# Optimization experiments

Measured on AMD Instinct MI355X. Metric: run time of the kernel, lower is better.

The kernel has to match this reference:

```python
import jax, jax.numpy as jnp
import numpy as np

EPS = 1e-9
C, Hd, Wd = 3, 64, 64  # input_dimensions[1:]

def setup_inputs() -> dict:
    key = jax.random.key(0)
    ks = jax.random.split(key, 8)
    S, B = 8, 512
    num_digits, num_style, num_hidden, bott, num_pixels = 10, 50, 512, 160, C * Hd * Wd
    return {
        "digits": jax.random.uniform(ks[0], (S, B, num_digits), dtype=jnp.float32),
        "styles": jax.random.normal(ks[1], (S, B, num_style), dtype=jnp.float32),
        "images": jax.random.uniform(ks[2], (S, B, C, Hd, Wd), dtype=jnp.float32),
        "W_h": jax.random.normal(ks[3], (num_digits + num_style, num_hidden), dtype=jnp.float32) * 0.05,
        "b_h": jnp.zeros((num_hidden,), jnp.float32),
        "W1": jax.random.normal(ks[4], (num_hidden, bott), dtype=jnp.float32) * 0.05,
        "b1": jnp.zeros((bott,), jnp.float32),
        "W2": jax.random.normal(ks[5], (bott, num_pixels), dtype=jnp.float32) * 0.05,
        "b2": jnp.zeros((num_pixels,), jnp.float32),
    }

def reference(digits, styles, images, W_h, b_h, W1, b1, W2, b2):
    # dec_hidden: Linear + ReLU, fully batched over [S, B]
    h = jax.nn.relu(jnp.concatenate([digits, styles], axis=-1) @ W_h + b_h)  # [S,B,Hn]
    # hidden_pass (original loops per-sample; here a single batched GEMM chain)
    t = jax.nn.selu(h @ W1 + b1)                 # [S,B,160]
    x_hat = jax.nn.sigmoid(t @ W2 + b2)          # [S,B,P]
    S, B, _ = x_hat.shape
    images_mean = x_hat.reshape(S, B, C, Hd, Wd)
    # eps-guarded BCE-style log-likelihood loss, summed over last dim only
    loss = -(jnp.log(images_mean + EPS) * images
             + jnp.log(1.0 - images_mean + EPS) * (1.0 - images)).sum(-1)  # [S,B,C,Hd]
    return loss
```

## Files before the change

kernel.cpp:

```cpp
#include <hip/hip_runtime.h>
#include <hip/hip_bf16.h>
#include <math.h>


#define SELU_SCALE 1.0507009873554804934193349852946f
#define SELU_ALPHA 1.6732632423543772848170429916717f

typedef __attribute__((ext_vector_type(8))) short bf16x8;
typedef __attribute__((ext_vector_type(4))) float f32x4;

static __device__ __forceinline__ short f2bf(float x) {
    __hip_bfloat16 h = __float2bfloat16(x);
    short s;
    __builtin_memcpy(&s, &h, 2);
    return s;
}

__global__ __launch_bounds__(512) void producer_kernel(
    const float* __restrict__ digits,
    const float* __restrict__ styles,
    const float* __restrict__ Wh,
    const float* __restrict__ bh,
    const float* __restrict__ W1,
    const float* __restrict__ b1,
    const float* __restrict__ W2,
    __hip_bfloat16* __restrict__ w2f,
    __hip_bfloat16* __restrict__ tf)
{
    __shared__ __align__(16) char smem[46912];
    const int tid = threadIdx.x;

    if (blockIdx.x < 256) {
        float (*cat_s)[60] = (float(*)[60])smem;
        float* h_s = (float*)(smem + 3840);
        float (*t_s)[161] = (float(*)[161])(smem + 3840 + 32768);
        const int rowBase = blockIdx.x * 16;

        for (int i = tid; i < 16 * 60; i += 512) {
            const int r = i / 60, k = i % 60;
            const int row = rowBase + r;
            cat_s[r][k] = (k < 10) ? digits[row * 10 + k]
                                   : styles[row * 50 + (k - 10)];
        }
        __syncthreads();

        {
            float acc[16];
            const float bias = bh[tid];
#pragma unroll
            for (int r = 0; r < 16; ++r) acc[r] = bias;
            for (int k = 0; k < 60; ++k) {
                const float w = Wh[k * 512 + tid];
#pragma unroll
                for (int r = 0; r < 16; ++r) acc[r] = fmaf(cat_s[r][k], w, acc[r]);
            }
#pragma unroll
            for (int r = 0; r < 16; ++r)
                h_s[r * 512 + tid] = fmaxf(acc[r], 0.0f);
        }
        __syncthreads();

        if (tid < 320) {
            const int rh = (tid >= 160) ? 1 : 0;
            const int col = tid - rh * 160;
            const int r0 = rh * 8;
            float acc[8];
            const float bias = b1[col];
#pragma unroll
            for (int r = 0; r < 8; ++r) acc[r] = bias;

#pragma unroll 4
            for (int k = 0; k < 512; k += 4) {
                const float w0 = W1[(size_t)(k + 0) * 160 + col];
                const float w1 = W1[(size_t)(k + 1) * 160 + col];
                const float w2 = W1[(size_t)(k + 2) * 160 + col];
                const float w3 = W1[(size_t)(k + 3) * 160 + col];
#pragma unroll
                for (int r = 0; r < 8; ++r) {
                    const float4 hv = *(const float4*)&h_s[(r0 + r) * 512 + k];
                    float a = acc[r];
                    a = fmaf(hv.x, w0, a);
                    a = fmaf(hv.y, w1, a);
                    a = fmaf(hv.z, w2, a);
                    a = fmaf(hv.w, w3, a);
                    acc[r] = a;
                }
            }
#pragma unroll
            for (int r = 0; r < 8; ++r) {
                const float z = acc[r];
                const float s = (z > 0.0f) ? (SELU_SCALE * z)
                                           : (SELU_SCALE * SELU_ALPHA * expm1f(z));
                t_s[r0 + r][col] = s;
            }
        }
        __syncthreads();

        if (tid < 320) {
            const int kk = tid >> 6;
            const int l = tid & 63;
            const int lr = l & 15, lh = l >> 4;
            bf16x8 v;
#pragma unroll
            for (int j = 0; j < 8; ++j)
                v[j] = f2bf(t_s[lr][kk * 32 + lh * 8 + j]);
            *(bf16x8*)((short*)tf + ((size_t)blockIdx.x * 5 + kk) * 512 + l * 8) = v;
        }
    } else {
        float (*tile)[64] = (float(*)[64])(smem + (tid >> 8) * 8192);
        const int p = (blockIdx.x - 256) * 2 + (tid >> 8);
        const int t256 = tid & 255;
        const int bx = p / 5, by = p % 5;
        const int colBase = bx * 64;
        const int kBase = by * 32;

        for (int i = t256; i < 32 * 64; i += 256)
            tile[i >> 6][i & 63] =
                W2[(size_t)(kBase + (i >> 6)) * 12288 + colBase + (i & 63)];
        __syncthreads();

        const int c16 = t256 >> 6;
        const int lane = t256 & 63;
        const int lr = lane & 15, lh = lane >> 4;

        bf16x8 v;
#pragma unroll
        for (int j = 0; j < 8; ++j)
            v[j] = f2bf(tile[lh * 8 + j][c16 * 16 + lr]);

        const size_t chunk = (size_t)(bx * 4 + c16) * 5 + by;
        *(bf16x8*)((short*)w2f + chunk * 512 + lane * 8) = v;
    }
}

__global__ __launch_bounds__(256, 3) void out_loss_mfma_kernel(
    const __hip_bfloat16* __restrict__ tf,
    const __hip_bfloat16* __restrict__ w2f,
    const float* __restrict__ b2,
    const float* __restrict__ images,
    float* __restrict__ out)
{
    __shared__ short w2s[20 * 512];
    __shared__ float ims[4][2048];

    const int tid = threadIdx.x;
    const int lane = tid & 63;
    const int wv = tid >> 6;
    const int rowBase = blockIdx.y * 128 + wv * 32;
    const int colBase = blockIdx.x * 64;
    const int lr = lane & 15;
    const int lh = lane >> 4;

    const short* wfb = (const short*)w2f;
    const short* tfb = (const short*)tf;
    const char* imb = (const char*)images;

    const int r16base = rowBase >> 4;
    bf16x8 bT[5][2];
#pragma unroll
    for (int kk = 0; kk < 5; ++kk)
#pragma unroll
        for (int r = 0; r < 2; ++r)
            bT[kk][r] = *(const bf16x8*)(tfb
                + ((size_t)(r16base + r) * 5 + kk) * 512 + lane * 8);
    float4 bc[4];
#pragma unroll
    for (int c = 0; c < 4; ++c)
        bc[c] = *(const float4*)(b2 + colBase + c * 16 + lh * 4);

    {
        const size_t chunkBase = (size_t)blockIdx.x * 20;
#pragma unroll
        for (int tch = 0; tch < 5; ++tch) {
            const int cw = wv + tch * 4;
            __builtin_amdgcn_global_load_lds(
                (const uint32_t*)(wfb + (chunkBase + cw) * 512 + lane * 8),
                (uint32_t*)&w2s[cw * 512], 16, 0, 0);
        }
    }
    {
        const int rsub = lane >> 4;
        const int m = lane & 15;
#pragma unroll
        for (int w = 0; w < 8; ++w) {
            const int r = w * 4 + rsub;
            const size_t gb = (size_t)(rowBase + r) * 49152 + (size_t)colBase * 4
                            + (size_t)((16 * m) ^ ((r & 15) << 4));
            __builtin_amdgcn_global_load_lds((const uint32_t*)(imb + gb),
                (uint32_t*)&ims[wv][w * 256], 16, 0, 0);
        }
    }

    asm volatile("s_waitcnt vmcnt(8)" ::: "memory");
    __builtin_amdgcn_sched_barrier(0);
    __builtin_amdgcn_s_barrier();

    f32x4 acc[4][2] = {};
#pragma unroll
    for (int kk = 0; kk < 5; ++kk) {
        bf16x8 aW[4];
#pragma unroll
        for (int c = 0; c < 4; ++c)
            aW[c] = *(const bf16x8*)&w2s[(c * 5 + kk) * 512 + lane * 8];
#pragma unroll
        for (int c = 0; c < 4; ++c)
#pragma unroll
            for (int r = 0; r < 2; ++r)
                acc[c][r] = __builtin_amdgcn_mfma_f32_16x16x32_bf16(
                    aW[c], bT[kk][r], acc[c][r], 0, 0, 0);
    }

    const float* myq = ims[wv];
#pragma unroll
    for (int rw = 0; rw < 2; ++rw) {
        if (rw == 0) {
            asm volatile("s_waitcnt vmcnt(4)" ::: "memory");
        } else {
            asm volatile("s_waitcnt vmcnt(0)" ::: "memory");
        }
        __builtin_amdgcn_sched_barrier(0);

        float mx = 0.f;
        float pr = 1.f;
        float zi = 0.f;
#pragma unroll
        for (int c = 0; c < 4; ++c) {
            const int fidx = (rw * 16 + lr) * 64 + ((lh * 4 + c * 16) ^ (lr << 2));
            const float4 im4 = *(const float4*)&myq[fidx];
            const float imv[4] = {im4.x, im4.y, im4.z, im4.w};
            const float bcv[4] = {bc[c].x, bc[c].y, bc[c].z, bc[c].w};
#pragma unroll
            for (int j = 0; j < 4; ++j) {
                const float z = acc[c][rw][j] + bcv[j];
                mx += fmaxf(z, 0.0f);
                pr *= 1.0f + __expf(-fabsf(z));
                zi = fmaf(z, imv[j], zi);
            }
        }
        float part = mx + __logf(pr) - zi;

        part += __shfl_xor(part, 16);
        part += __shfl_xor(part, 32);

        if (lane < 16)
            out[(size_t)(rowBase + rw * 16 + lane) * 192 + blockIdx.x] = part;
    }
}

extern "C" void kernel_launch(void* const* d_in, const int* in_sizes, int n_in,
                              void* d_out, int out_size, void* d_ws, size_t ws_size,
                              hipStream_t stream) {
    const float* digits = (const float*)d_in[0];
    const float* styles = (const float*)d_in[1];
    const float* images = (const float*)d_in[2];
    const float* Wh     = (const float*)d_in[3];
    const float* bh     = (const float*)d_in[4];
    const float* W1     = (const float*)d_in[5];
    const float* b1     = (const float*)d_in[6];
    const float* W2     = (const float*)d_in[7];
    const float* b2     = (const float*)d_in[8];
    float* out = (float*)d_out;

    __hip_bfloat16* w2f = (__hip_bfloat16*)d_ws;
    __hip_bfloat16* tf  = w2f + (size_t)12288 * 160;

    producer_kernel<<<736, 512, 0, stream>>>(digits, styles, Wh, bh, W1, b1,
                                             W2, w2f, tf);

    dim3 grid3(192, 32);
    out_loss_mfma_kernel<<<grid3, 256, 0, stream>>>(tf, w2f, b2, images, out);
}
```

Before: 82.59 us.

## Double-buffer image and activation loads across four row iterations per block

Each block now covers 256 rows instead of 128, with each wave processing four 16-row slices in a loop. Image tiles and activation fragments are double-buffered so the loads for slices two steps ahead are issued while the current slice computes. The W2 tile held in LDS is reused across more rows, and the grid shrinks by half. This trades fewer blocks and tighter vmcnt bookkeeping for better overlap of memory traffic with MFMA and loss math.

```diff
diff --git a/kernel.cpp b/kernel.cpp
--- a/kernel.cpp
+++ b/kernel.cpp
@@ -141,13 +141,13 @@
     float* __restrict__ out)
 {
     __shared__ short w2s[20 * 512];
-    __shared__ float ims[4][2048];
+    __shared__ float ims[4][2][1024];
 
     const int tid = threadIdx.x;
     const int lane = tid & 63;
     const int wv = tid >> 6;
-    const int rowBase = blockIdx.y * 128 + wv * 32;
-    const int colBase = blockIdx.x * 64;
+    const int colBlk = blockIdx.x;
+    const int colBase = colBlk * 64;
     const int lr = lane & 15;
     const int lh = lane >> 4;
 
@@ -155,21 +155,42 @@
     const short* tfb = (const short*)tf;
     const char* imb = (const char*)images;
 
-    const int r16base = rowBase >> 4;
-    bf16x8 bT[5][2];
-#pragma unroll
-    for (int kk = 0; kk < 5; ++kk)
-#pragma unroll
-        for (int r = 0; r < 2; ++r)
-            bT[kk][r] = *(const bf16x8*)(tfb
-                + ((size_t)(r16base + r) * 5 + kk) * 512 + lane * 8);
+    const int rsub = lane >> 4;
+    const int m16 = lane & 15;
+
+    const int rowW = blockIdx.y * 256 + wv * 16;
+
+#define ISSUE_IMS(it_, slot_)                                                  \
+    {                                                                          \
+        const int rb = rowW + (it_) * 64;                                      \
+        _Pragma("unroll")                                                      \
+        for (int w = 0; w < 4; ++w) {                                          \
+            const int r = w * 4 + rsub;                                        \
+            const size_t gb = (size_t)(rb + r) * 49152 + (size_t)colBase * 4   \
+                            + (size_t)((16 * m16) ^ ((r & 15) << 4));          \
+            __builtin_amdgcn_global_load_lds((const uint32_t*)(imb + gb),      \
+                (uint32_t*)&ims[wv][slot_][w * 256], 16, 0, 0);                \
+        }                                                                      \
+    }
+
+#define ISSUE_BT(it_, bank_)                                                   \
+    {                                                                          \
+        const int r16 = (rowW + (it_) * 64) >> 4;                              \
+        _Pragma("unroll")                                                      \
+        for (int kk = 0; kk < 5; ++kk)                                         \
+            bT[bank_][kk] = *(const bf16x8*)(tfb                               \
+                + ((size_t)r16 * 5 + kk) * 512 + lane * 8);                    \
+    }
+
+    bf16x8 bT[2][5];
+
     float4 bc[4];
 #pragma unroll
     for (int c = 0; c < 4; ++c)
         bc[c] = *(const float4*)(b2 + colBase + c * 16 + lh * 4);
-
+    ISSUE_BT(0, 0)
     {
-        const size_t chunkBase = (size_t)blockIdx.x * 20;
+        const size_t chunkBase = (size_t)colBlk * 20;
 #pragma unroll
         for (int tch = 0; tch < 5; ++tch) {
             const int cw = wv + tch * 4;
@@ -178,73 +199,86 @@
                 (uint32_t*)&w2s[cw * 512], 16, 0, 0);
         }
     }
-    {
-        const int rsub = lane >> 4;
-        const int m = lane & 15;
-#pragma unroll
-        for (int w = 0; w < 8; ++w) {
-            const int r = w * 4 + rsub;
-            const size_t gb = (size_t)(rowBase + r) * 49152 + (size_t)colBase * 4
-                            + (size_t)((16 * m) ^ ((r & 15) << 4));
-            __builtin_amdgcn_global_load_lds((const uint32_t*)(imb + gb),
-                (uint32_t*)&ims[wv][w * 256], 16, 0, 0);
-        }
-    }
-
-    asm volatile("s_waitcnt vmcnt(8)" ::: "memory");
+    ISSUE_IMS(0, 0)
+    ISSUE_BT(1, 1)
+    ISSUE_IMS(1, 1)
+
+    asm volatile("s_waitcnt vmcnt(9)" ::: "memory");
     __builtin_amdgcn_sched_barrier(0);
     __builtin_amdgcn_s_barrier();
 
-    f32x4 acc[4][2] = {};
-#pragma unroll
-    for (int kk = 0; kk < 5; ++kk) {
-        bf16x8 aW[4];
-#pragma unroll
-        for (int c = 0; c < 4; ++c)
-            aW[c] = *(const bf16x8*)&w2s[(c * 5 + kk) * 512 + lane * 8];
-#pragma unroll
-        for (int c = 0; c < 4; ++c)
-#pragma unroll
-            for (int r = 0; r < 2; ++r)
-                acc[c][r] = __builtin_amdgcn_mfma_f32_16x16x32_bf16(
-                    aW[c], bT[kk][r], acc[c][r], 0, 0, 0);
-    }
-
-    const float* myq = ims[wv];
-#pragma unroll
-    for (int rw = 0; rw < 2; ++rw) {
-        if (rw == 0) {
-            asm volatile("s_waitcnt vmcnt(4)" ::: "memory");
-        } else {
-            asm volatile("s_waitcnt vmcnt(0)" ::: "memory");
-        }
+    float parts[4];
+
+#pragma unroll
+    for (int it = 0; it < 4; ++it) {
+        if (it >= 1) {
+            if (it < 3) {
+                asm volatile("s_waitcnt vmcnt(9)" ::: "memory");
+            } else {
+                asm volatile("s_waitcnt vmcnt(0)" ::: "memory");
+            }
+            __builtin_amdgcn_sched_barrier(0);
+        }
+
+        f32x4 acc[4] = {};
+#pragma unroll
+        for (int kk = 0; kk < 5; ++kk) {
+            bf16x8 aW[4];
+#pragma unroll
+            for (int c = 0; c < 4; ++c)
+                aW[c] = *(const bf16x8*)&w2s[(c * 5 + kk) * 512 + lane * 8];
+#pragma unroll
+            for (int c = 0; c < 4; ++c)
+                acc[c] = __builtin_amdgcn_mfma_f32_16x16x32_bf16(
+                    aW[c], bT[it & 1][kk], acc[c], 0, 0, 0);
+        }
+
+        float4 img[4];
+#pragma unroll
+        for (int c = 0; c < 4; ++c) {
+            const int fidx = lr * 64 + ((lh * 4 + c * 16) ^ (lr << 2));
+            img[c] = *(const float4*)&ims[wv][it & 1][fidx];
+        }
+        asm volatile("s_waitcnt lgkmcnt(0)" ::: "memory");
         __builtin_amdgcn_sched_barrier(0);
+
+        if (it < 2) {
+            ISSUE_BT(it + 2, it & 1)
+            ISSUE_IMS(it + 2, it & 1)
+        }
 
         float mx = 0.f;
         float pr = 1.f;
         float zi = 0.f;
 #pragma unroll
         for (int c = 0; c < 4; ++c) {
-            const int fidx = (rw * 16 + lr) * 64 + ((lh * 4 + c * 16) ^ (lr << 2));
-            const float4 im4 = *(const float4*)&myq[fidx];
-            const float imv[4] = {im4.x, im4.y, im4.z, im4.w};
+            const float imv[4] = {img[c].x, img[c].y, img[c].z, img[c].w};
             const float bcv[4] = {bc[c].x, bc[c].y, bc[c].z, bc[c].w};
 #pragma unroll
             for (int j = 0; j < 4; ++j) {
-                const float z = acc[c][rw][j] + bcv[j];
+                const float z = acc[c][j] + bcv[j];
                 mx += fmaxf(z, 0.0f);
                 pr *= 1.0f + __expf(-fabsf(z));
                 zi = fmaf(z, imv[j], zi);
             }
         }
         float part = mx + __logf(pr) - zi;
-
         part += __shfl_xor(part, 16);
         part += __shfl_xor(part, 32);
 
-        if (lane < 16)
-            out[(size_t)(rowBase + rw * 16 + lane) * 192 + blockIdx.x] = part;
-    }
+        if (it == 0)      parts[0] = part;
+        else if (it == 1) parts[1] = part;
+        else if (it == 2) parts[2] = part;
+        else              parts[3] = part;
+    }
+
+    if (lane < 16) {
+#pragma unroll
+        for (int it = 0; it < 4; ++it)
+            out[(size_t)(rowW + it * 64 + lane) * 192 + colBlk] = parts[it];
+    }
+#undef ISSUE_IMS
+#undef ISSUE_BT
 }
 
 extern "C" void kernel_launch(void* const* d_in, const int* in_sizes, int n_in,
@@ -267,6 +301,6 @@
     producer_kernel<<<736, 512, 0, stream>>>(digits, styles, Wh, bh, W1, b1,
                                              W2, w2f, tf);
 
-    dim3 grid3(192, 32);
+    dim3 grid3(192, 16);
     out_loss_mfma_kernel<<<grid3, 256, 0, stream>>>(tf, w2f, b2, images, out);
 }
```

Measured after the change: 80.43 us. 2.6% less time.
